# Optimization experiments

Measured on AMD Instinct MI355X. Metric: run time of the kernel, lower is better.

## Reference

```python
import jax, jax.numpy as jnp
import numpy as np

B, S, D_IN, H, SS, D_OUT = 4, 4096, 2048, 32, 64, 2048


def setup_inputs() -> dict:
    key = jax.random.key(0)
    k1, k2, k3, k4, k5 = jax.random.split(key, 5)
    x = jax.random.normal(k1, (B, S, D_IN), dtype=jnp.float32)
    input_state = jnp.zeros((B, H, SS), dtype=jnp.float32)
    input_weight = jax.random.normal(k2, (H * SS, D_IN), dtype=jnp.float32) * 0.02
    state_weight = jax.random.normal(k3, (H, SS, SS), dtype=jnp.float32) * 0.05
    state_bias = jax.random.normal(k4, (H, SS), dtype=jnp.float32) * 0.02
    output_weight = jax.random.normal(k5, (D_OUT, H * SS), dtype=jnp.float32) * 0.02
    return {
        "x": x,
        "input_state": input_state,
        "input_weight": input_weight,
        "state_weight": state_weight,
        "state_bias": state_bias,
        "output_weight": output_weight,
    }


def reference(x, input_state, input_weight, state_weight, state_bias, output_weight):
    b, s, _ = x.shape
    h, ss, _ = state_weight.shape
    # input projection: [B,S,D_in] -> [B,S,H,Ss], bias folded in once
    hx = jnp.einsum("bsi,oi->bso", x, input_weight).reshape(b, s, h, ss) + state_bias

    def step(y_prev, h_t):
        # y_t = tanh(W_state @ y_{t-1} + x_t)   per head
        y = jnp.tanh(jnp.einsum("hij,bhj->bhi", state_weight, y_prev) + h_t)
        return y, y

    # scan over time axis
    _, ys = jax.lax.scan(step, input_state, jnp.transpose(hx, (1, 0, 2, 3)))
    y = jnp.transpose(ys, (1, 0, 2, 3)).reshape(b, s, h * ss)
    return jnp.einsum("bsk,ok->bso", y, output_weight)
```

## Files before the change

### kernel.cpp

```cpp
#include <hip/hip_runtime.h>
#include <hip/hip_bf16.h>
#include <stdint.h>

#define S_LEN 4096
#define HN    32
#define SSD   64
#define KD    2048
#define MROWS 16384

typedef __attribute__((ext_vector_type(4))) float f32x4;
typedef __attribute__((ext_vector_type(8))) short bf16x8;
typedef __attribute__((ext_vector_type(2))) int i32x2;
typedef __attribute__((ext_vector_type(2))) _Float16 f16x2;
typedef __attribute__((address_space(3))) char as3char;
typedef __attribute__((address_space(1))) char as1char;

__device__ __forceinline__ unsigned short f2bf(float f){
  unsigned int u = __float_as_uint(f);
  u += 0x7FFFu + ((u >> 16) & 1u);
  return (unsigned short)(u >> 16);
}

__device__ __forceinline__ f16x2 bc_h2(int v){
  union { int i; f16x2 h; } u; u.i = v; return u.h;
}

__global__ __launch_bounds__(256) void cvt_bf16_k(const float* __restrict__ src,
                                                  unsigned short* __restrict__ dst){
  int i = (blockIdx.x * 256 + threadIdx.x) * 4;
  float4 v = *(const float4*)(src + i);
  ushort4 r;
  r.x = f2bf(v.x); r.y = f2bf(v.y); r.z = f2bf(v.z); r.w = f2bf(v.w);
  *(ushort4*)(dst + i) = r;
}

__global__ __launch_bounds__(256) void gemm_bf16_k(const unsigned short* __restrict__ A,
                                                   const unsigned short* __restrict__ Bw,
                                                   const float* __restrict__ bias,
                                                   float* __restrict__ C){
  __shared__ short As[128*32];
  __shared__ short Bs[128*32];
  const int tid  = threadIdx.x;
  const int bn   = blockIdx.x & 15;
  const int bm   = blockIdx.x >> 4;
  const int lane = tid & 63;
  const int wv   = tid >> 6;
  const int wvU  = __builtin_amdgcn_readfirstlane(wv);
  const int wm   = (wv >> 1) * 64;
  const int wn   = (wv & 1) * 64;

  f32x4 acc[4][4];
#pragma unroll
  for (int i=0;i<4;i++)
#pragma unroll
    for (int j=0;j<4;j++)
#pragma unroll
      for (int q=0;q<4;q++) acc[i][j][q] = 0.0f;

  as3char* asB = (as3char*)As;
  as3char* bsB = (as3char*)Bs;
  as1char* aG  = (as1char*)A;
  as1char* bG  = (as1char*)Bw;

  const int fr  = lane & 15;
  const int fko = (lane >> 4) * 8;

  for (int kt=0; kt<KD/32; ++kt){
    __syncthreads();
#pragma unroll
    for (int c=0;c<2;c++){
      const int off  = (wvU*2 + c)*1024 + lane*16;
      const int row  = off >> 6;
      const int colB = off & 63;
      __builtin_amdgcn_global_load_lds(
        (__attribute__((address_space(1))) void*)(aG + (size_t)(bm*128 + row)*4096 + (size_t)kt*64 + colB),
        (__attribute__((address_space(3))) void*)(asB + (wvU*2 + c)*1024),
        16, 0, 0);
      __builtin_amdgcn_global_load_lds(
        (__attribute__((address_space(1))) void*)(bG + (size_t)(bn*128 + row)*4096 + (size_t)kt*64 + colB),
        (__attribute__((address_space(3))) void*)(bsB + (wvU*2 + c)*1024),
        16, 0, 0);
    }
    __syncthreads();

    bf16x8 af[4], bq[4];
#pragma unroll
    for (int mt=0; mt<4; mt++) af[mt] = *(const bf16x8*)&As[(wm + mt*16 + fr)*32 + fko];
#pragma unroll
    for (int nt=0; nt<4; nt++) bq[nt] = *(const bf16x8*)&Bs[(wn + nt*16 + fr)*32 + fko];
#pragma unroll
    for (int mt=0; mt<4; mt++)
#pragma unroll
      for (int nt=0; nt<4; nt++)
        acc[mt][nt] = __builtin_amdgcn_mfma_f32_16x16x32_bf16(af[mt], bq[nt], acc[mt][nt], 0, 0, 0);
  }

  float bv[4] = {0.f, 0.f, 0.f, 0.f};
  if (bias){
#pragma unroll
    for (int nt=0; nt<4; nt++) bv[nt] = bias[bn*128 + wn + nt*16 + fr];
  }
#pragma unroll
  for (int mt=0; mt<4; mt++)
#pragma unroll
    for (int nt=0; nt<4; nt++){
      const int col = bn*128 + wn + nt*16 + fr;
#pragma unroll
      for (int q=0; q<4; q++){
        const int row = bm*128 + wm + mt*16 + (lane>>4)*4 + q;
        C[(size_t)row*KD + col] = acc[mt][nt][q] + bv[nt];
      }
    }
}

__global__ __attribute__((amdgpu_flat_work_group_size(64, 64)))
__attribute__((amdgpu_waves_per_eu(1, 1)))
void scan_k(const float* __restrict__ hx,
            const float* __restrict__ sw,
            const float* __restrict__ st0,
            unsigned short* __restrict__ ybf){
  const int b = blockIdx.x >> 5, h = blockIdx.x & 31;
  const int lane = threadIdx.x;
  const f32x4* wv = (const f32x4*)(sw + ((size_t)(h*64 + lane))*64);

#define MKP(Q, PA, PB) { f32x4 q_ = wv[Q]; \
    PA = f16x2{(_Float16)q_[0], (_Float16)q_[1]}; \
    PB = f16x2{(_Float16)q_[2], (_Float16)q_[3]}; }
  f16x2 p0,p1,p2,p3,p4,p5,p6,p7,p8,p9,p10,p11,p12,p13,p14,p15,
        p16,p17,p18,p19,p20,p21,p22,p23,p24,p25,p26,p27,p28,p29,p30,p31;
  MKP(0,p0,p1)   MKP(1,p2,p3)   MKP(2,p4,p5)   MKP(3,p6,p7)
  MKP(4,p8,p9)   MKP(5,p10,p11) MKP(6,p12,p13) MKP(7,p14,p15)
  MKP(8,p16,p17) MKP(9,p18,p19) MKP(10,p20,p21)MKP(11,p22,p23)
  MKP(12,p24,p25)MKP(13,p26,p27)MKP(14,p28,p29)MKP(15,p30,p31)
#undef MKP
  asm volatile("" : "+v"(p0),"+v"(p1),"+v"(p2),"+v"(p3),"+v"(p4),"+v"(p5),
                    "+v"(p6),"+v"(p7),"+v"(p8),"+v"(p9),"+v"(p10),"+v"(p11),
                    "+v"(p12),"+v"(p13),"+v"(p14),"+v"(p15));
  asm volatile("" : "+v"(p16),"+v"(p17),"+v"(p18),"+v"(p19),"+v"(p20),"+v"(p21),
                    "+v"(p22),"+v"(p23),"+v"(p24),"+v"(p25),"+v"(p26),"+v"(p27),
                    "+v"(p28),"+v"(p29),"+v"(p30),"+v"(p31));

  __shared__ __align__(16) unsigned short ybuf[4][64];

  float y = st0[(b*32 + h)*64 + lane];
  const float* hxp = hx + (size_t)b*S_LEN*KD + h*64 + lane;
  unsigned short* const ybase = ybf + (size_t)b*S_LEN*KD + h*64;
  const int srow = lane >> 4;
  const int scol = (lane & 15) << 2;

  unsigned hb0 = (unsigned)__builtin_bit_cast(unsigned short, (_Float16)y);
  int nb0 = __builtin_amdgcn_update_dpp(0, (int)hb0, 0xB1, 0xF, 0xF, true);
  int yp = (int)(hb0 | ((unsigned)nb0 << 16));

  float h0 = hxp[0*(size_t)KD], h1 = hxp[1*(size_t)KD],
        h2 = hxp[2*(size_t)KD], h3 = hxp[3*(size_t)KD];

#define DOT8(G, P0,P1,P2,P3,P4,P5,P6,P7) { \
    const int t0 = __builtin_amdgcn_readlane(yp, (G)*16+ 0); \
    const int t1 = __builtin_amdgcn_readlane(yp, (G)*16+ 2); \
    const int t2 = __builtin_amdgcn_readlane(yp, (G)*16+ 4); \
    const int t3 = __builtin_amdgcn_readlane(yp, (G)*16+ 6); \
    const int t4 = __builtin_amdgcn_readlane(yp, (G)*16+ 8); \
    const int t5 = __builtin_amdgcn_readlane(yp, (G)*16+10); \
    const int t6 = __builtin_amdgcn_readlane(yp, (G)*16+12); \
    const int t7 = __builtin_amdgcn_readlane(yp, (G)*16+14); \
    __builtin_amdgcn_sched_barrier(0); \
    a0 = __builtin_amdgcn_fdot2(P0, bc_h2(t0), a0, false); \
    a1 = __builtin_amdgcn_fdot2(P1, bc_h2(t1), a1, false); \
    a2 = __builtin_amdgcn_fdot2(P2, bc_h2(t2), a2, false); \
    a3 = __builtin_amdgcn_fdot2(P3, bc_h2(t3), a3, false); \
    a0 = __builtin_amdgcn_fdot2(P4, bc_h2(t4), a0, false); \
    a1 = __builtin_amdgcn_fdot2(P5, bc_h2(t5), a1, false); \
    a2 = __builtin_amdgcn_fdot2(P6, bc_h2(t6), a2, false); \
    a3 = __builtin_amdgcn_fdot2(P7, bc_h2(t7), a3, false); \
    __builtin_amdgcn_sched_barrier(0); }

#define RNN_STEP(H, J, TT) { \
    const float hxv = H; \
    { const int tn_ = ((TT) + 4 < S_LEN) ? ((TT) + 4) : (S_LEN - 1); \
      H = hxp[(size_t)tn_ * KD]; } \
    float a0=0.f, a1=0.f, a2=0.f, a3=0.f; \
    DOT8(0, p0,p1,p2,p3,p4,p5,p6,p7) \
    DOT8(1, p8,p9,p10,p11,p12,p13,p14,p15) \
    DOT8(2, p16,p17,p18,p19,p20,p21,p22,p23) \
    DOT8(3, p24,p25,p26,p27,p28,p29,p30,p31) \
    const float u = (a0 + a1) + (a2 + a3) + hxv; \
    const float e = __expf(2.0f*u); \
    y = 1.0f - 2.0f*__builtin_amdgcn_rcpf(e + 1.0f); \
    ybuf[J][lane] = f2bf(y); \
    { const unsigned hb = (unsigned)__builtin_bit_cast(unsigned short, (_Float16)y); \
      const int nb = __builtin_amdgcn_update_dpp(0, (int)hb, 0xB1, 0xF, 0xF, true); \
      yp = (int)(hb | ((unsigned)nb << 16)); } }

  for (int t = 0; t < S_LEN; t += 4){
    RNN_STEP(h0, 0, t+0)
    RNN_STEP(h1, 1, t+1)
    RNN_STEP(h2, 2, t+2)
    RNN_STEP(h3, 3, t+3)
    const i32x2 v = *(const i32x2*)&ybuf[srow][scol];
    *(i32x2*)(ybase + (size_t)(t + srow)*KD + scol) = v;
  }
#undef RNN_STEP
#undef DOT8
}

extern "C" void kernel_launch(void* const* d_in, const int* in_sizes, int n_in,
                              void* d_out, int out_size, void* d_ws, size_t ws_size,
                              hipStream_t stream) {
  const float* x      = (const float*)d_in[0];
  const float* st0    = (const float*)d_in[1];
  const float* w_in   = (const float*)d_in[2];
  const float* w_st   = (const float*)d_in[3];
  const float* b_st   = (const float*)d_in[4];
  const float* w_out  = (const float*)d_in[5];
  float* out = (float*)d_out;

  const size_t HX_B = (size_t)MROWS * KD * 4;
  const size_t Y_B  = (size_t)MROWS * KD * 2;
  const size_t WO_B = (size_t)KD * KD * 2;
  if (ws_size < HX_B + Y_B + WO_B) return;
  char* ws = (char*)d_ws;
  float*          hx   = (float*)ws;
  unsigned short* ybf  = (unsigned short*)(ws + HX_B);
  unsigned short* wbf  = (unsigned short*)(ws + HX_B + Y_B);

  cvt_bf16_k<<<dim3((MROWS*(size_t)KD)/1024), dim3(256), 0, stream>>>(x, ybf);
  cvt_bf16_k<<<dim3((KD*KD)/1024), dim3(256), 0, stream>>>(w_in, wbf);
  gemm_bf16_k<<<dim3((MROWS/128)*(KD/128)), dim3(256), 0, stream>>>(ybf, wbf, b_st, hx);
  scan_k<<<dim3(128), dim3(64), 0, stream>>>(hx, w_st, st0, ybf);
  cvt_bf16_k<<<dim3((KD*KD)/1024), dim3(256), 0, stream>>>(w_out, wbf);
  gemm_bf16_k<<<dim3((MROWS/128)*(KD/128)), dim3(256), 0, stream>>>(ybf, wbf, nullptr, out);
}
```

Before: 1.201 ms.

## Interleave four batch recurrences per scan wavefront to hide latency

```diff
diff --git a/kernel.cpp b/kernel.cpp
--- a/kernel.cpp
+++ b/kernel.cpp
@@ -23,6 +23,12 @@
 
 __device__ __forceinline__ f16x2 bc_h2(int v){
   union { int i; f16x2 h; } u; u.i = v; return u.h;
+}
+
+__device__ __forceinline__ int packpair(float y){
+  const unsigned hb = (unsigned)__builtin_bit_cast(unsigned short, (_Float16)y);
+  const int nb = __builtin_amdgcn_update_dpp(0, (int)hb, 0xB1, 0xF, 0xF, true);
+  return (int)(hb | ((unsigned)nb << 16));
 }
 
 __global__ __launch_bounds__(256) void cvt_bf16_k(const float* __restrict__ src,
@@ -119,7 +125,7 @@
             const float* __restrict__ sw,
             const float* __restrict__ st0,
             unsigned short* __restrict__ ybf){
-  const int b = blockIdx.x >> 5, h = blockIdx.x & 31;
+  const int h = blockIdx.x;
   const int lane = threadIdx.x;
   const f32x4* wv = (const f32x4*)(sw + ((size_t)(h*64 + lane))*64);
 
@@ -140,68 +146,98 @@
                     "+v"(p22),"+v"(p23),"+v"(p24),"+v"(p25),"+v"(p26),"+v"(p27),
                     "+v"(p28),"+v"(p29),"+v"(p30),"+v"(p31));
 
-  __shared__ __align__(16) unsigned short ybuf[4][64];
-
-  float y = st0[(b*32 + h)*64 + lane];
-  const float* hxp = hx + (size_t)b*S_LEN*KD + h*64 + lane;
-  unsigned short* const ybase = ybf + (size_t)b*S_LEN*KD + h*64;
+  __shared__ __align__(16) unsigned short ybuf[4][4][64];
+
+  float yA = st0[(0*32 + h)*64 + lane];
+  float yB = st0[(1*32 + h)*64 + lane];
+  float yC = st0[(2*32 + h)*64 + lane];
+  float yD = st0[(3*32 + h)*64 + lane];
+  int ypA = packpair(yA), ypB = packpair(yB), ypC = packpair(yC), ypD = packpair(yD);
+
+  const float* hxpA = hx + (size_t)0*S_LEN*KD + h*64 + lane;
+  const float* hxpB = hx + (size_t)1*S_LEN*KD + h*64 + lane;
+  const float* hxpC = hx + (size_t)2*S_LEN*KD + h*64 + lane;
+  const float* hxpD = hx + (size_t)3*S_LEN*KD + h*64 + lane;
+  unsigned short* const ybA = ybf + (size_t)0*S_LEN*KD + h*64;
+  unsigned short* const ybB = ybf + (size_t)1*S_LEN*KD + h*64;
+  unsigned short* const ybC = ybf + (size_t)2*S_LEN*KD + h*64;
+  unsigned short* const ybD = ybf + (size_t)3*S_LEN*KD + h*64;
   const int srow = lane >> 4;
   const int scol = (lane & 15) << 2;
 
-  unsigned hb0 = (unsigned)__builtin_bit_cast(unsigned short, (_Float16)y);
-  int nb0 = __builtin_amdgcn_update_dpp(0, (int)hb0, 0xB1, 0xF, 0xF, true);
-  int yp = (int)(hb0 | ((unsigned)nb0 << 16));
-
-  float h0 = hxp[0*(size_t)KD], h1 = hxp[1*(size_t)KD],
-        h2 = hxp[2*(size_t)KD], h3 = hxp[3*(size_t)KD];
-
-#define DOT8(G, P0,P1,P2,P3,P4,P5,P6,P7) { \
-    const int t0 = __builtin_amdgcn_readlane(yp, (G)*16+ 0); \
-    const int t1 = __builtin_amdgcn_readlane(yp, (G)*16+ 2); \
-    const int t2 = __builtin_amdgcn_readlane(yp, (G)*16+ 4); \
-    const int t3 = __builtin_amdgcn_readlane(yp, (G)*16+ 6); \
-    const int t4 = __builtin_amdgcn_readlane(yp, (G)*16+ 8); \
-    const int t5 = __builtin_amdgcn_readlane(yp, (G)*16+10); \
-    const int t6 = __builtin_amdgcn_readlane(yp, (G)*16+12); \
-    const int t7 = __builtin_amdgcn_readlane(yp, (G)*16+14); \
+  float hA0=hxpA[0*(size_t)KD], hA1=hxpA[1*(size_t)KD], hA2=hxpA[2*(size_t)KD], hA3=hxpA[3*(size_t)KD];
+  float hB0=hxpB[0*(size_t)KD], hB1=hxpB[1*(size_t)KD], hB2=hxpB[2*(size_t)KD], hB3=hxpB[3*(size_t)KD];
+  float hC0=hxpC[0*(size_t)KD], hC1=hxpC[1*(size_t)KD], hC2=hxpC[2*(size_t)KD], hC3=hxpC[3*(size_t)KD];
+  float hD0=hxpD[0*(size_t)KD], hD1=hxpD[1*(size_t)KD], hD2=hxpD[2*(size_t)KD], hD3=hxpD[3*(size_t)KD];
+
+#define RL8(C, G) \
+    const int t##C##0=__builtin_amdgcn_readlane(yp##C,(G)*16+ 0); \
+    const int t##C##1=__builtin_amdgcn_readlane(yp##C,(G)*16+ 2); \
+    const int t##C##2=__builtin_amdgcn_readlane(yp##C,(G)*16+ 4); \
+    const int t##C##3=__builtin_amdgcn_readlane(yp##C,(G)*16+ 6); \
+    const int t##C##4=__builtin_amdgcn_readlane(yp##C,(G)*16+ 8); \
+    const int t##C##5=__builtin_amdgcn_readlane(yp##C,(G)*16+10); \
+    const int t##C##6=__builtin_amdgcn_readlane(yp##C,(G)*16+12); \
+    const int t##C##7=__builtin_amdgcn_readlane(yp##C,(G)*16+14);
+
+#define DT8(C, P0,P1,P2,P3,P4,P5,P6,P7) \
+    a##C##0=__builtin_amdgcn_fdot2(P0,bc_h2(t##C##0),a##C##0,false); \
+    a##C##1=__builtin_amdgcn_fdot2(P1,bc_h2(t##C##1),a##C##1,false); \
+    a##C##2=__builtin_amdgcn_fdot2(P2,bc_h2(t##C##2),a##C##2,false); \
+    a##C##3=__builtin_amdgcn_fdot2(P3,bc_h2(t##C##3),a##C##3,false); \
+    a##C##0=__builtin_amdgcn_fdot2(P4,bc_h2(t##C##4),a##C##0,false); \
+    a##C##1=__builtin_amdgcn_fdot2(P5,bc_h2(t##C##5),a##C##1,false); \
+    a##C##2=__builtin_amdgcn_fdot2(P6,bc_h2(t##C##6),a##C##2,false); \
+    a##C##3=__builtin_amdgcn_fdot2(P7,bc_h2(t##C##7),a##C##3,false);
+
+#define GRP(G, P0,P1,P2,P3,P4,P5,P6,P7) { \
+    RL8(A, G) RL8(B, G) RL8(C, G) RL8(D, G) \
     __builtin_amdgcn_sched_barrier(0); \
-    a0 = __builtin_amdgcn_fdot2(P0, bc_h2(t0), a0, false); \
-    a1 = __builtin_amdgcn_fdot2(P1, bc_h2(t1), a1, false); \
-    a2 = __builtin_amdgcn_fdot2(P2, bc_h2(t2), a2, false); \
-    a3 = __builtin_amdgcn_fdot2(P3, bc_h2(t3), a3, false); \
-    a0 = __builtin_amdgcn_fdot2(P4, bc_h2(t4), a0, false); \
-    a1 = __builtin_amdgcn_fdot2(P5, bc_h2(t5), a1, false); \
-    a2 = __builtin_amdgcn_fdot2(P6, bc_h2(t6), a2, false); \
-    a3 = __builtin_amdgcn_fdot2(P7, bc_h2(t7), a3, false); \
+    DT8(A, P0,P1,P2,P3,P4,P5,P6,P7) \
+    DT8(B, P0,P1,P2,P3,P4,P5,P6,P7) \
+    DT8(C, P0,P1,P2,P3,P4,P5,P6,P7) \
+    DT8(D, P0,P1,P2,P3,P4,P5,P6,P7) \
     __builtin_amdgcn_sched_barrier(0); }
 
-#define RNN_STEP(H, J, TT) { \
-    const float hxv = H; \
-    { const int tn_ = ((TT) + 4 < S_LEN) ? ((TT) + 4) : (S_LEN - 1); \
-      H = hxp[(size_t)tn_ * KD]; } \
-    float a0=0.f, a1=0.f, a2=0.f, a3=0.f; \
-    DOT8(0, p0,p1,p2,p3,p4,p5,p6,p7) \
-    DOT8(1, p8,p9,p10,p11,p12,p13,p14,p15) \
-    DOT8(2, p16,p17,p18,p19,p20,p21,p22,p23) \
-    DOT8(3, p24,p25,p26,p27,p28,p29,p30,p31) \
-    const float u = (a0 + a1) + (a2 + a3) + hxv; \
+#define FIN(C, CI, XV, J) { \
+    const float u = (a##C##0 + a##C##1) + (a##C##2 + a##C##3) + (XV); \
     const float e = __expf(2.0f*u); \
-    y = 1.0f - 2.0f*__builtin_amdgcn_rcpf(e + 1.0f); \
-    ybuf[J][lane] = f2bf(y); \
-    { const unsigned hb = (unsigned)__builtin_bit_cast(unsigned short, (_Float16)y); \
-      const int nb = __builtin_amdgcn_update_dpp(0, (int)hb, 0xB1, 0xF, 0xF, true); \
-      yp = (int)(hb | ((unsigned)nb << 16)); } }
+    y##C = 1.0f - 2.0f*__builtin_amdgcn_rcpf(e + 1.0f); \
+    ybuf[CI][J][lane] = f2bf(y##C); \
+    yp##C = packpair(y##C); }
+
+#define STEP4(HA_,HB_,HC_,HD_, J, TT) { \
+    const float xvA=HA_, xvB=HB_, xvC=HC_, xvD=HD_; \
+    { const int tn_ = ((TT)+4 < S_LEN) ? ((TT)+4) : (S_LEN-1); \
+      HA_ = hxpA[(size_t)tn_*KD]; HB_ = hxpB[(size_t)tn_*KD]; \
+      HC_ = hxpC[(size_t)tn_*KD]; HD_ = hxpD[(size_t)tn_*KD]; } \
+    float aA0=0.f,aA1=0.f,aA2=0.f,aA3=0.f, aB0=0.f,aB1=0.f,aB2=0.f,aB3=0.f; \
+    float aC0=0.f,aC1=0.f,aC2=0.f,aC3=0.f, aD0=0.f,aD1=0.f,aD2=0.f,aD3=0.f; \
+    GRP(0, p0,p1,p2,p3,p4,p5,p6,p7) \
+    GRP(1, p8,p9,p10,p11,p12,p13,p14,p15) \
+    GRP(2, p16,p17,p18,p19,p20,p21,p22,p23) \
+    GRP(3, p24,p25,p26,p27,p28,p29,p30,p31) \
+    FIN(A, 0, xvA, J) FIN(B, 1, xvB, J) FIN(C, 2, xvC, J) FIN(D, 3, xvD, J) }
 
   for (int t = 0; t < S_LEN; t += 4){
-    RNN_STEP(h0, 0, t+0)
-    RNN_STEP(h1, 1, t+1)
-    RNN_STEP(h2, 2, t+2)
-    RNN_STEP(h3, 3, t+3)
-    const i32x2 v = *(const i32x2*)&ybuf[srow][scol];
-    *(i32x2*)(ybase + (size_t)(t + srow)*KD + scol) = v;
+    STEP4(hA0,hB0,hC0,hD0, 0, t+0)
+    STEP4(hA1,hB1,hC1,hD1, 1, t+1)
+    STEP4(hA2,hB2,hC2,hD2, 2, t+2)
+    STEP4(hA3,hB3,hC3,hD3, 3, t+3)
+    { const i32x2 v = *(const i32x2*)&ybuf[0][srow][scol];
+      *(i32x2*)(ybA + (size_t)(t + srow)*KD + scol) = v; }
+    { const i32x2 v = *(const i32x2*)&ybuf[1][srow][scol];
+      *(i32x2*)(ybB + (size_t)(t + srow)*KD + scol) = v; }
+    { const i32x2 v = *(const i32x2*)&ybuf[2][srow][scol];
+      *(i32x2*)(ybC + (size_t)(t + srow)*KD + scol) = v; }
+    { const i32x2 v = *(const i32x2*)&ybuf[3][srow][scol];
+      *(i32x2*)(ybD + (size_t)(t + srow)*KD + scol) = v; }
   }
-#undef RNN_STEP
-#undef DOT8
+#undef STEP4
+#undef FIN
+#undef GRP
+#undef DT8
+#undef RL8
 }
 
 extern "C" void kernel_launch(void* const* d_in, const int* in_sizes, int n_in,
@@ -227,7 +263,7 @@
   cvt_bf16_k<<<dim3((MROWS*(size_t)KD)/1024), dim3(256), 0, stream>>>(x, ybf);
   cvt_bf16_k<<<dim3((KD*KD)/1024), dim3(256), 0, stream>>>(w_in, wbf);
   gemm_bf16_k<<<dim3((MROWS/128)*(KD/128)), dim3(256), 0, stream>>>(ybf, wbf, b_st, hx);
-  scan_k<<<dim3(128), dim3(64), 0, stream>>>(hx, w_st, st0, ybf);
+  scan_k<<<dim3(HN), dim3(64), 0, stream>>>(hx, w_st, st0, ybf);
   cvt_bf16_k<<<dim3((KD*KD)/1024), dim3(256), 0, stream>>>(w_out, wbf);
   gemm_bf16_k<<<dim3((MROWS/128)*(KD/128)), dim3(256), 0, stream>>>(ybf, wbf, nullptr, out);
 }
```

New measurement: 3.290 ms. 2.74x slower.
